# Optimization experiments

Measured on AMD Instinct MI355X. Metric: run time of the kernel, lower is better.

The kernel has to match this reference:

```python
import jax, jax.numpy as jnp
import numpy as np

B, N, D, H, DK, DV = 16, 512, 512, 8, 64, 64


def setup_inputs() -> dict:
    key = jax.random.key(0)
    ks = jax.random.split(key, 16)
    xav = lambda k, fi, fo: jax.random.uniform(k, (fi, fo), jnp.float32,
                                               -jnp.sqrt(6.0 / (fi + fo)), jnp.sqrt(6.0 / (fi + fo)))
    return {
        "queries": jax.random.normal(ks[0], (B, N, D), jnp.float32),
        "keys": jax.random.normal(ks[1], (B, N, D), jnp.float32),
        "values": jax.random.normal(ks[2], (B, N, D), jnp.float32),
        "box_relation_embed_matrix": jax.random.uniform(ks[3], (B, H, N, N), jnp.float32),
        "ExtrAtt": jax.random.normal(ks[4], (B, H, N, N), jnp.float32),
        "Wq": xav(ks[5], D, H * DK), "bq": jnp.zeros((H * DK,), jnp.float32),
        "Wk": xav(ks[6], D, H * DK), "bk": jnp.zeros((H * DK,), jnp.float32),
        "Wv": xav(ks[7], D, H * DV), "bv": jnp.zeros((H * DV,), jnp.float32),
        "Wo": xav(ks[8], H * DV, D), "bo": jnp.zeros((D,), jnp.float32),
    }


def reference(queries, keys, values, box_relation_embed_matrix, ExtrAtt,
              Wq, bq, Wk, bk, Wv, bv, Wo, bo):
    b_s, nq, _ = queries.shape
    nk = keys.shape[1]
    # projections -> [B, H, N, d]
    q = (queries @ Wq + bq).reshape(b_s, nq, H, DK).transpose(0, 2, 1, 3)
    k = (keys @ Wk + bk).reshape(b_s, nk, H, DK).transpose(0, 2, 1, 3)
    v = (values @ Wv + bv).reshape(b_s, nk, H, DV).transpose(0, 2, 1, 3)
    scale = 1.0 / jnp.sqrt(jnp.asarray(DK, queries.dtype))
    att = jnp.einsum('bhqd,bhkd->bhqk', q, k) * scale
    # log geometric (box) bias + content attention, first softmax
    w_mn = jnp.log(jnp.clip(box_relation_embed_matrix, 1e-6, None)) + att
    w_mn = jax.nn.softmax(w_mn, axis=-1)
    # dropout is identity in eval; add extra attention and re-normalize
    att2 = jax.nn.softmax(w_mn + ExtrAtt, axis=-1)
    out = jnp.einsum('bhqk,bhkd->bhqd', att2, v)
    out = out.transpose(0, 2, 1, 3).reshape(b_s, nq, H * DV)
    return out @ Wo + bo
```

## Files before the change

kernel.cpp:

```cpp
#include <hip/hip_runtime.h>
#include <hip/hip_bf16.h>

#define NB 16
#define NN 512
#define ND 512
#define NH 8

using short8 = __attribute__((ext_vector_type(8))) short;
using f32x4  = __attribute__((ext_vector_type(4))) float;

static __device__ __forceinline__ unsigned short f2bf(float f) {
  unsigned u = __builtin_bit_cast(unsigned, f);
  unsigned r = 0x7fffu + ((u >> 16) & 1u);
  return (unsigned short)((u + r) >> 16);
}
static __device__ __forceinline__ float bf2f(unsigned short u) {
  return __builtin_bit_cast(float, (unsigned)u << 16);
}
static __device__ __forceinline__ void ld_lds16(const float* g, float* l) {
  __builtin_amdgcn_global_load_lds((const __attribute__((address_space(1))) void*)g,
                                   (__attribute__((address_space(3))) void*)l, 16, 0, 0);
}

__global__ __launch_bounds__(256) void wprep(
    const float* __restrict__ Wq, const float* __restrict__ Wk,
    const float* __restrict__ Wv, const float* __restrict__ Wo,
    unsigned short* __restrict__ T) {
  const float* W;
  switch (blockIdx.z) {
    case 0: W = Wq; break;
    case 1: W = Wk; break;
    case 2: W = Wv; break;
    default: W = Wo; break;
  }
  unsigned short* Wt = T + (size_t)blockIdx.z * 512 * 512;
  __shared__ float tile[64][65];
  const int t = threadIdx.x;
  const int k0 = blockIdx.x * 64, n0 = blockIdx.y * 64;
#pragma unroll
  for (int it = 0; it < 4; ++it) {
    int row = it * 16 + (t >> 4);
    int c4 = (t & 15) * 4;
    float4 v = *(const float4*)&W[(size_t)(k0 + row) * 512 + n0 + c4];
    tile[row][c4] = v.x; tile[row][c4 + 1] = v.y;
    tile[row][c4 + 2] = v.z; tile[row][c4 + 3] = v.w;
  }
  __syncthreads();
#pragma unroll
  for (int it = 0; it < 4; ++it) {
    int nr = it * 16 + (t >> 4);
    int k4 = (t & 15) * 4;
    ushort4 o;
    o.x = f2bf(tile[k4 + 0][nr]); o.y = f2bf(tile[k4 + 1][nr]);
    o.z = f2bf(tile[k4 + 2][nr]); o.w = f2bf(tile[k4 + 3][nr]);
    *(ushort4*)&Wt[(size_t)(n0 + nr) * 512 + k0 + k4] = o;
  }
}

__global__ __launch_bounds__(256) void qkv_gemm(
    const float* __restrict__ Xq, const float* __restrict__ Xk,
    const float* __restrict__ Xv, const unsigned short* __restrict__ Wt,
    const float* __restrict__ bq, const float* __restrict__ bk,
    const float* __restrict__ bv, unsigned short* __restrict__ q_ws,
    unsigned short* __restrict__ k_ws, unsigned short* __restrict__ vt_ws) {
  const int zi = blockIdx.z;
  const float* X = (zi == 0) ? Xq : (zi == 1) ? Xk : Xv;
  const unsigned short* Wz = Wt + (size_t)zi * 512 * 512;
  const float* bias = (zi == 0) ? bq : (zi == 1) ? bk : bv;
  const int m0 = blockIdx.x * 128, n0 = blockIdx.y * 128;
  __shared__ unsigned short Al[2][128][40];
  __shared__ unsigned short Bl[2][128][40];
  const int t = threadIdx.x;
  const int w = t >> 6, l = t & 63;
  const int lr = l & 15, lg = l >> 4;
  const int wr = (w >> 1) * 64, wc = (w & 1) * 64;
  f32x4 acc[4][4] = {};
  for (int kk = 0; kk < 512; kk += 64) {
    __syncthreads();
    {
      const int colk = (t & 15) * 4;
      const int kc = colk >> 5, kin = colk & 31;
#pragma unroll
      for (int p = 0; p < 8; ++p) {
        int row = p * 16 + (t >> 4);
        float4 v = *(const float4*)&X[(size_t)(m0 + row) * 512 + kk + colk];
        ushort4 o;
        o.x = f2bf(v.x); o.y = f2bf(v.y); o.z = f2bf(v.z); o.w = f2bf(v.w);
        *(ushort4*)&Al[kc][row][kin] = o;
      }
      const int colk8 = (t & 7) * 8;
      const int kc2 = colk8 >> 5, kin2 = colk8 & 31;
#pragma unroll
      for (int p = 0; p < 4; ++p) {
        int row = p * 32 + (t >> 3);
        short8 v = *(const short8*)&Wz[(size_t)(n0 + row) * 512 + kk + colk8];
        *(short8*)&Bl[kc2][row][kin2] = v;
      }
    }
    __syncthreads();
#pragma unroll
    for (int kc = 0; kc < 2; ++kc) {
      short8 a[4], b[4];
      const int lk = lg * 8;
#pragma unroll
      for (int i = 0; i < 4; ++i) a[i] = *(const short8*)&Al[kc][wr + i * 16 + lr][lk];
#pragma unroll
      for (int i = 0; i < 4; ++i) b[i] = *(const short8*)&Bl[kc][wc + i * 16 + lr][lk];
#pragma unroll
      for (int i = 0; i < 4; ++i)
#pragma unroll
        for (int j = 0; j < 4; ++j)
          acc[i][j] = __builtin_amdgcn_mfma_f32_16x16x32_bf16(a[i], b[j], acc[i][j], 0, 0, 0);
    }
  }
#pragma unroll
  for (int j = 0; j < 4; ++j) {
    const int col = n0 + wc + j * 16 + lr;
    const float bb = bias[col];
    const int hh = col >> 6, dv = col & 63;
#pragma unroll
    for (int i = 0; i < 4; ++i) {
      const int mbase = m0 + wr + i * 16 + lg * 4;
      const int b_ = mbase >> 9, nt = mbase & 511;
      if (zi == 2) {
        ushort4 o;
        o.x = f2bf(acc[i][j][0] + bb); o.y = f2bf(acc[i][j][1] + bb);
        o.z = f2bf(acc[i][j][2] + bb); o.w = f2bf(acc[i][j][3] + bb);
        *(ushort4*)&vt_ws[((size_t)(b_ * NH + hh) * 64 + dv) * 512 + nt] = o;
      } else {
        unsigned short* dst = (zi == 0) ? q_ws : k_ws;
#pragma unroll
        for (int r = 0; r < 4; ++r)
          dst[((size_t)(b_ * NH + hh) * 512 + nt + r) * 64 + dv] = f2bf(acc[i][j][r] + bb);
      }
    }
  }
}

__global__ __launch_bounds__(256, 3) void attn_kernel(
    const unsigned short* __restrict__ q_ws, const unsigned short* __restrict__ k_ws,
    const unsigned short* __restrict__ vt_ws, const float* __restrict__ box,
    const float* __restrict__ Ext, unsigned short* __restrict__ hidden) {
  const int t = threadIdx.x;
  const int w = t >> 6, l = t & 63;
  const int lr = l & 15, lg = l >> 4;
  const int bh = blockIdx.y;
  const int q0 = blockIdx.x * 16;
  const int b = bh >> 3, h = bh & 7;

  const unsigned short* Qp = q_ws + (size_t)bh * 512 * 64;
  const unsigned short* Kp = k_ws + (size_t)bh * 512 * 64;
  const unsigned short* Vt = vt_ws + (size_t)bh * 64 * 512;
  const float* boxp = box + ((size_t)bh * 512 + q0) * 512;
  const float* Ep = Ext + ((size_t)bh * 512 + q0) * 512;

  __shared__ float stg[4][2048];
  __shared__ unsigned short Pt[4][16][144];
  __shared__ float red[4][16];
  __shared__ float red2[4][16];

  const int n0w = w * 128;
  float* wst = stg[w];
  unsigned short(*Pw)[144] = Pt[w];

  short8 qf0 = *(const short8*)&Qp[(size_t)(q0 + lr) * 64 + lg * 8];
  short8 qf1 = *(const short8*)&Qp[(size_t)(q0 + lr) * 64 + 32 + lg * 8];
  short8 kf[8][2];
#pragma unroll
  for (int c = 0; c < 8; ++c) {
    const int krow = n0w + c * 16 + lr;
    kf[c][0] = *(const short8*)&Kp[(size_t)krow * 64 + lg * 8];
    kf[c][1] = *(const short8*)&Kp[(size_t)krow * 64 + 32 + lg * 8];
  }
#pragma unroll
  for (int it = 0; it < 8; ++it) {
    const int row2 = it * 2 + (l >> 5);
    const int slot = (l & 31) ^ (row2 & 7);
    ld_lds16(&boxp[(size_t)row2 * 512 + n0w + slot * 4], &wst[it * 256]);
  }
  __builtin_amdgcn_sched_barrier(0);

  f32x4 z[8];
#pragma unroll
  for (int c = 0; c < 8; ++c) {
    f32x4 a = {0.f, 0.f, 0.f, 0.f};
    a = __builtin_amdgcn_mfma_f32_16x16x32_bf16(kf[c][0], qf0, a, 0, 0, 0);
    a = __builtin_amdgcn_mfma_f32_16x16x32_bf16(kf[c][1], qf1, a, 0, 0, 0);
    z[c] = a;
  }
  asm volatile("s_waitcnt vmcnt(0)" ::: "memory");

  float s1 = 0.f;
#pragma unroll
  for (int c = 0; c < 8; ++c) {
    f32x4 bx4 = *(const f32x4*)&wst[lr * 128 + (((c * 4 + lg) ^ (lr & 7)) << 2)];
    ushort4 o;
    float e0 = fmaxf(bx4[0], 1e-6f) * __expf(z[c][0] * 0.125f);
    float e1 = fmaxf(bx4[1], 1e-6f) * __expf(z[c][1] * 0.125f);
    float e2 = fmaxf(bx4[2], 1e-6f) * __expf(z[c][2] * 0.125f);
    float e3 = fmaxf(bx4[3], 1e-6f) * __expf(z[c][3] * 0.125f);
    s1 += (e0 + e1) + (e2 + e3);
    o.x = f2bf(e0); o.y = f2bf(e1); o.z = f2bf(e2); o.w = f2bf(e3);
    *(ushort4*)&Pw[lr][c * 16 + lg * 4] = o;
  }
  asm volatile("s_waitcnt lgkmcnt(0)" ::: "memory");
#pragma unroll
  for (int it = 0; it < 8; ++it) {
    const int row2 = it * 2 + (l >> 5);
    const int slot = (l & 31) ^ (row2 & 7);
    ld_lds16(&Ep[(size_t)row2 * 512 + n0w + slot * 4], &wst[it * 256]);
  }
  __builtin_amdgcn_sched_barrier(0);
  s1 += __shfl_xor(s1, 16);
  s1 += __shfl_xor(s1, 32);
  if (lg == 0) red[w][lr] = s1;
  asm volatile("s_waitcnt lgkmcnt(0)" ::: "memory");
  __builtin_amdgcn_s_barrier();
  const float l1i = 1.0f / (red[0][lr] + red[1][lr] + red[2][lr] + red[3][lr]);
  asm volatile("s_waitcnt vmcnt(0)" ::: "memory");

  float s2 = 0.f;
#pragma unroll
  for (int c = 0; c < 8; ++c) {
    f32x4 ex4 = *(const f32x4*)&wst[lr * 128 + (((c * 4 + lg) ^ (lr & 7)) << 2)];
    ushort4 u = *(const ushort4*)&Pw[lr][c * 16 + lg * 4];
    ushort4 o;
    float e0 = __expf(bf2f(u.x) * l1i + ex4[0]);
    float e1 = __expf(bf2f(u.y) * l1i + ex4[1]);
    float e2 = __expf(bf2f(u.z) * l1i + ex4[2]);
    float e3 = __expf(bf2f(u.w) * l1i + ex4[3]);
    s2 += (e0 + e1) + (e2 + e3);
    o.x = f2bf(e0); o.y = f2bf(e1); o.z = f2bf(e2); o.w = f2bf(e3);
    *(ushort4*)&Pw[lr][c * 16 + lg * 4] = o;
  }
  s2 += __shfl_xor(s2, 16);
  s2 += __shfl_xor(s2, 32);
  if (lg == 0) red2[w][lr] = s2;
  asm volatile("s_waitcnt lgkmcnt(0)" ::: "memory");
  __builtin_amdgcn_s_barrier();

  f32x4 o4[4] = {};
#pragma unroll
  for (int kc = 0; kc < 4; ++kc) {
    short8 pa = *(const short8*)&Pw[lr][kc * 32 + lg * 8];
#pragma unroll
    for (int c2 = 0; c2 < 4; ++c2) {
      short8 vf = *(const short8*)&Vt[(size_t)(c2 * 16 + lr) * 512 + n0w + kc * 32 + lg * 8];
      o4[c2] = __builtin_amdgcn_mfma_f32_16x16x32_bf16(pa, vf, o4[c2], 0, 0, 0);
    }
  }
  f32x4 rs = *(const f32x4*)&red2[0][lg * 4];
#pragma unroll
  for (int w2 = 1; w2 < 4; ++w2) {
    f32x4 p = *(const f32x4*)&red2[w2][lg * 4];
#pragma unroll
    for (int r = 0; r < 4; ++r) rs[r] += p[r];
  }
  f32x4 l2v;
#pragma unroll
  for (int r = 0; r < 4; ++r) l2v[r] = 1.0f / rs[r];
  float* ow = (float*)Pw;
#pragma unroll
  for (int c2 = 0; c2 < 4; ++c2)
#pragma unroll
    for (int r = 0; r < 4; ++r)
      ow[(lg * 4 + r) * 68 + c2 * 16 + lr] = o4[c2][r] * l2v[r];
  asm volatile("s_waitcnt lgkmcnt(0)" ::: "memory");
  __builtin_amdgcn_s_barrier();
  {
    const int lrow = t >> 4;
    const int d4 = (t & 15) * 4;
    f32x4 s = *(const f32x4*)&((const float*)Pt[0])[lrow * 68 + d4];
#pragma unroll
    for (int w2 = 1; w2 < 4; ++w2) {
      f32x4 p = *(const f32x4*)&((const float*)Pt[w2])[lrow * 68 + d4];
#pragma unroll
      for (int r = 0; r < 4; ++r) s[r] += p[r];
    }
    ushort4 oo;
    oo.x = f2bf(s[0]); oo.y = f2bf(s[1]); oo.z = f2bf(s[2]); oo.w = f2bf(s[3]);
    *(ushort4*)&hidden[(size_t)(b * 512 + q0 + lrow) * 512 + h * 64 + d4] = oo;
  }
}

__global__ __launch_bounds__(256) void out_gemm(
    const unsigned short* __restrict__ hidden, const unsigned short* __restrict__ WoT,
    const float* __restrict__ bo, float* __restrict__ out) {
  const int m0 = blockIdx.x * 128, n0 = blockIdx.y * 128;
  __shared__ unsigned short Al[2][128][40];
  __shared__ unsigned short Bl[2][128][40];
  const int t = threadIdx.x;
  const int w = t >> 6, l = t & 63;
  const int lr = l & 15, lg = l >> 4;
  const int wr = (w >> 1) * 64, wc = (w & 1) * 64;
  f32x4 acc[4][4] = {};
  for (int kk = 0; kk < 512; kk += 64) {
    __syncthreads();
    {
      const int colk8 = (t & 7) * 8;
      const int kc2 = colk8 >> 5, kin2 = colk8 & 31;
#pragma unroll
      for (int p = 0; p < 4; ++p) {
        int row = p * 32 + (t >> 3);
        short8 v = *(const short8*)&hidden[(size_t)(m0 + row) * 512 + kk + colk8];
        *(short8*)&Al[kc2][row][kin2] = v;
      }
#pragma unroll
      for (int p = 0; p < 4; ++p) {
        int row = p * 32 + (t >> 3);
        short8 v = *(const short8*)&WoT[(size_t)(n0 + row) * 512 + kk + colk8];
        *(short8*)&Bl[kc2][row][kin2] = v;
      }
    }
    __syncthreads();
#pragma unroll
    for (int kc = 0; kc < 2; ++kc) {
      short8 a[4], b[4];
      const int lk = lg * 8;
#pragma unroll
      for (int i = 0; i < 4; ++i) a[i] = *(const short8*)&Al[kc][wr + i * 16 + lr][lk];
#pragma unroll
      for (int i = 0; i < 4; ++i) b[i] = *(const short8*)&Bl[kc][wc + i * 16 + lr][lk];
#pragma unroll
      for (int i = 0; i < 4; ++i)
#pragma unroll
        for (int j = 0; j < 4; ++j)
          acc[i][j] = __builtin_amdgcn_mfma_f32_16x16x32_bf16(a[i], b[j], acc[i][j], 0, 0, 0);
    }
  }
#pragma unroll
  for (int j = 0; j < 4; ++j) {
    const int col = n0 + wc + j * 16 + lr;
    const float bb = bo[col];
#pragma unroll
    for (int i = 0; i < 4; ++i)
#pragma unroll
      for (int r = 0; r < 4; ++r)
        out[(size_t)(m0 + wr + i * 16 + lg * 4 + r) * 512 + col] = acc[i][j][r] + bb;
  }
}

extern "C" void kernel_launch(void* const* d_in, const int* in_sizes, int n_in,
                              void* d_out, int out_size, void* d_ws, size_t ws_size,
                              hipStream_t stream) {
  const float* queries = (const float*)d_in[0];
  const float* keys = (const float*)d_in[1];
  const float* values = (const float*)d_in[2];
  const float* box = (const float*)d_in[3];
  const float* ext = (const float*)d_in[4];
  const float* Wq = (const float*)d_in[5];
  const float* bq = (const float*)d_in[6];
  const float* Wk = (const float*)d_in[7];
  const float* bk = (const float*)d_in[8];
  const float* Wv = (const float*)d_in[9];
  const float* bv = (const float*)d_in[10];
  const float* Wo = (const float*)d_in[11];
  const float* bo = (const float*)d_in[12];
  float* out = (float*)d_out;

  char* ws = (char*)d_ws;
  unsigned short* q_ws = (unsigned short*)(ws);
  unsigned short* k_ws = (unsigned short*)(ws + 8u * 1024 * 1024);
  unsigned short* vt_ws = (unsigned short*)(ws + 16u * 1024 * 1024);
  unsigned short* hidden = (unsigned short*)(ws + 24u * 1024 * 1024);
  unsigned short* wt = (unsigned short*)(ws + 32u * 1024 * 1024);

  wprep<<<dim3(8, 8, 4), 256, 0, stream>>>(Wq, Wk, Wv, Wo, wt);
  qkv_gemm<<<dim3(64, 4, 3), 256, 0, stream>>>(queries, keys, values, wt, bq, bk, bv,
                                               q_ws, k_ws, vt_ws);
  attn_kernel<<<dim3(32, 128), 256, 0, stream>>>(q_ws, k_ws, vt_ws, box, ext, hidden);
  out_gemm<<<dim3(64, 4), 256, 0, stream>>>(hidden, wt + 3u * 512 * 512, bo, out);
}
```

Measured before the change: 157.4 us.

## Prefetch box and ExtrAtt tiles together and remap blocks to XCDs

Issues the LDS loads for both the box tile and the ExtrAtt tile up front, each into its own staging buffer, and waits only for the box loads before the first softmax. The ExtrAtt fetch then overlaps the first exp pass. The LDS tile layout changes to a chunked, unswizzled form, and P now aliases the box region. The launch becomes a 1D grid where workgroup id modulo 8 selects the head group so each XCD keeps the same (b,h) K/V data in its L2. LDS per block doubles and occupancy is lowered to 2 blocks per CU, and dropping the swizzle may add bank conflicts.

```diff
diff --git a/kernel.cpp b/kernel.cpp
--- a/kernel.cpp
+++ b/kernel.cpp
@@ -137,15 +137,17 @@
   }
 }
 
-__global__ __launch_bounds__(256, 3) void attn_kernel(
+__global__ __launch_bounds__(256, 2) void attn_kernel(
     const unsigned short* __restrict__ q_ws, const unsigned short* __restrict__ k_ws,
     const unsigned short* __restrict__ vt_ws, const float* __restrict__ box,
     const float* __restrict__ Ext, unsigned short* __restrict__ hidden) {
   const int t = threadIdx.x;
   const int w = t >> 6, l = t & 63;
   const int lr = l & 15, lg = l >> 4;
-  const int bh = blockIdx.y;
-  const int q0 = blockIdx.x * 16;
+  const int wg = blockIdx.x;
+  const int xcd = wg & 7, slot = wg >> 3;
+  const int bh = xcd + 8 * (slot >> 5);
+  const int q0 = (slot & 31) * 16;
   const int b = bh >> 3, h = bh & 7;
 
   const unsigned short* Qp = q_ws + (size_t)bh * 512 * 64;
@@ -154,14 +156,14 @@
   const float* boxp = box + ((size_t)bh * 512 + q0) * 512;
   const float* Ep = Ext + ((size_t)bh * 512 + q0) * 512;
 
-  __shared__ float stg[4][2048];
-  __shared__ unsigned short Pt[4][16][144];
+  __shared__ __align__(16) unsigned char stg[4][16384];
   __shared__ float red[4][16];
   __shared__ float red2[4][16];
 
   const int n0w = w * 128;
-  float* wst = stg[w];
-  unsigned short(*Pw)[144] = Pt[w];
+  float* wst = (float*)stg[w];
+  float* wstE = (float*)(stg[w] + 8192);
+  unsigned short* Pus = (unsigned short*)stg[w];
 
   short8 qf0 = *(const short8*)&Qp[(size_t)(q0 + lr) * 64 + lg * 8];
   short8 qf1 = *(const short8*)&Qp[(size_t)(q0 + lr) * 64 + 32 + lg * 8];
@@ -172,12 +174,13 @@
     kf[c][0] = *(const short8*)&Kp[(size_t)krow * 64 + lg * 8];
     kf[c][1] = *(const short8*)&Kp[(size_t)krow * 64 + 32 + lg * 8];
   }
-#pragma unroll
-  for (int it = 0; it < 8; ++it) {
-    const int row2 = it * 2 + (l >> 5);
-    const int slot = (l & 31) ^ (row2 & 7);
-    ld_lds16(&boxp[(size_t)row2 * 512 + n0w + slot * 4], &wst[it * 256]);
-  }
+  __builtin_amdgcn_sched_barrier(0);
+#pragma unroll
+  for (int c = 0; c < 8; ++c)
+    ld_lds16(&boxp[(size_t)(l >> 2) * 512 + n0w + c * 16 + (l & 3) * 4], &wst[c * 256]);
+#pragma unroll
+  for (int c = 0; c < 8; ++c)
+    ld_lds16(&Ep[(size_t)(l >> 2) * 512 + n0w + c * 16 + (l & 3) * 4], &wstE[c * 256]);
   __builtin_amdgcn_sched_barrier(0);
 
   f32x4 z[8];
@@ -188,29 +191,22 @@
     a = __builtin_amdgcn_mfma_f32_16x16x32_bf16(kf[c][1], qf1, a, 0, 0, 0);
     z[c] = a;
   }
-  asm volatile("s_waitcnt vmcnt(0)" ::: "memory");
+  asm volatile("s_waitcnt vmcnt(8)" ::: "memory");
+  __builtin_amdgcn_sched_barrier(0);
 
   float s1 = 0.f;
 #pragma unroll
   for (int c = 0; c < 8; ++c) {
-    f32x4 bx4 = *(const f32x4*)&wst[lr * 128 + (((c * 4 + lg) ^ (lr & 7)) << 2)];
-    ushort4 o;
+    f32x4 bx4 = *(const f32x4*)&wst[c * 256 + lr * 16 + lg * 4];
     float e0 = fmaxf(bx4[0], 1e-6f) * __expf(z[c][0] * 0.125f);
     float e1 = fmaxf(bx4[1], 1e-6f) * __expf(z[c][1] * 0.125f);
     float e2 = fmaxf(bx4[2], 1e-6f) * __expf(z[c][2] * 0.125f);
     float e3 = fmaxf(bx4[3], 1e-6f) * __expf(z[c][3] * 0.125f);
     s1 += (e0 + e1) + (e2 + e3);
+    ushort4 o;
     o.x = f2bf(e0); o.y = f2bf(e1); o.z = f2bf(e2); o.w = f2bf(e3);
-    *(ushort4*)&Pw[lr][c * 16 + lg * 4] = o;
-  }
-  asm volatile("s_waitcnt lgkmcnt(0)" ::: "memory");
-#pragma unroll
-  for (int it = 0; it < 8; ++it) {
-    const int row2 = it * 2 + (l >> 5);
-    const int slot = (l & 31) ^ (row2 & 7);
-    ld_lds16(&Ep[(size_t)row2 * 512 + n0w + slot * 4], &wst[it * 256]);
-  }
-  __builtin_amdgcn_sched_barrier(0);
+    *(ushort4*)&Pus[c * 256 + lr * 16 + lg * 4] = o;
+  }
   s1 += __shfl_xor(s1, 16);
   s1 += __shfl_xor(s1, 32);
   if (lg == 0) red[w][lr] = s1;
@@ -218,20 +214,21 @@
   __builtin_amdgcn_s_barrier();
   const float l1i = 1.0f / (red[0][lr] + red[1][lr] + red[2][lr] + red[3][lr]);
   asm volatile("s_waitcnt vmcnt(0)" ::: "memory");
+  __builtin_amdgcn_sched_barrier(0);
 
   float s2 = 0.f;
 #pragma unroll
   for (int c = 0; c < 8; ++c) {
-    f32x4 ex4 = *(const f32x4*)&wst[lr * 128 + (((c * 4 + lg) ^ (lr & 7)) << 2)];
-    ushort4 u = *(const ushort4*)&Pw[lr][c * 16 + lg * 4];
-    ushort4 o;
+    f32x4 ex4 = *(const f32x4*)&wstE[c * 256 + lr * 16 + lg * 4];
+    ushort4 u = *(const ushort4*)&Pus[c * 256 + lr * 16 + lg * 4];
     float e0 = __expf(bf2f(u.x) * l1i + ex4[0]);
     float e1 = __expf(bf2f(u.y) * l1i + ex4[1]);
     float e2 = __expf(bf2f(u.z) * l1i + ex4[2]);
     float e3 = __expf(bf2f(u.w) * l1i + ex4[3]);
     s2 += (e0 + e1) + (e2 + e3);
+    ushort4 o;
     o.x = f2bf(e0); o.y = f2bf(e1); o.z = f2bf(e2); o.w = f2bf(e3);
-    *(ushort4*)&Pw[lr][c * 16 + lg * 4] = o;
+    *(ushort4*)&Pus[c * 256 + lr * 16 + lg * 4] = o;
   }
   s2 += __shfl_xor(s2, 16);
   s2 += __shfl_xor(s2, 32);
@@ -242,7 +239,7 @@
   f32x4 o4[4] = {};
 #pragma unroll
   for (int kc = 0; kc < 4; ++kc) {
-    short8 pa = *(const short8*)&Pw[lr][kc * 32 + lg * 8];
+    short8 pa = *(const short8*)&Pus[(kc * 2 + (lg >> 1)) * 256 + lr * 16 + (lg & 1) * 8];
 #pragma unroll
     for (int c2 = 0; c2 < 4; ++c2) {
       short8 vf = *(const short8*)&Vt[(size_t)(c2 * 16 + lr) * 512 + n0w + kc * 32 + lg * 8];
@@ -259,7 +256,7 @@
   f32x4 l2v;
 #pragma unroll
   for (int r = 0; r < 4; ++r) l2v[r] = 1.0f / rs[r];
-  float* ow = (float*)Pw;
+  float* ow = (float*)stg[w];
 #pragma unroll
   for (int c2 = 0; c2 < 4; ++c2)
 #pragma unroll
@@ -270,10 +267,10 @@
   {
     const int lrow = t >> 4;
     const int d4 = (t & 15) * 4;
-    f32x4 s = *(const f32x4*)&((const float*)Pt[0])[lrow * 68 + d4];
+    f32x4 s = *(const f32x4*)&((const float*)stg[0])[lrow * 68 + d4];
 #pragma unroll
     for (int w2 = 1; w2 < 4; ++w2) {
-      f32x4 p = *(const f32x4*)&((const float*)Pt[w2])[lrow * 68 + d4];
+      f32x4 p = *(const f32x4*)&((const float*)stg[w2])[lrow * 68 + d4];
 #pragma unroll
       for (int r = 0; r < 4; ++r) s[r] += p[r];
     }
@@ -368,6 +365,6 @@
   wprep<<<dim3(8, 8, 4), 256, 0, stream>>>(Wq, Wk, Wv, Wo, wt);
   qkv_gemm<<<dim3(64, 4, 3), 256, 0, stream>>>(queries, keys, values, wt, bq, bk, bv,
                                                q_ws, k_ws, vt_ws);
-  attn_kernel<<<dim3(32, 128), 256, 0, stream>>>(q_ws, k_ws, vt_ws, box, ext, hidden);
+  attn_kernel<<<dim3(4096), 256, 0, stream>>>(q_ws, k_ws, vt_ws, box, ext, hidden);
   out_gemm<<<dim3(64, 4), 256, 0, stream>>>(hidden, wt + 3u * 512 * 512, bo, out);
 }
```

Result: slower. 164.6 us (+4.6%).
